# Kernel tuning notes

Measured on AMD Instinct MI355X. Metric: run time of the kernel, lower is better.

The kernel has to match this reference:

```python
import jax, jax.numpy as jnp
import numpy as np

N = 50000      # nodes
E = 800000     # edges (before self-loops)
F_IN = 128     # input features
HID = 64       # hidden width
CLS = 40       # classes
NEG_SLOPE = 0.2  # PyG GATConv default
EPS = 1e-16


def setup_inputs() -> dict:
    key = jax.random.key(0)
    ks = jax.random.split(key, 16)

    def lin(k, fi, fo):
        return jax.random.normal(k, (fi, fo), jnp.float32) / np.float32(np.sqrt(fi))

    def att(k, f):
        return jax.random.normal(k, (f,), jnp.float32) / np.float32(np.sqrt(f))

    return {
        "x": jax.random.normal(ks[0], (N, F_IN), jnp.float32),
        "edge_index": jax.random.randint(ks[1], (2, E), 0, N, dtype=jnp.int64),
        "W1": lin(ks[2], F_IN, HID), "a_src1": att(ks[3], HID), "a_dst1": att(ks[4], HID), "b1": jnp.zeros((HID,), jnp.float32),
        "W2": lin(ks[5], HID, HID),  "a_src2": att(ks[6], HID), "a_dst2": att(ks[7], HID), "b2": jnp.zeros((HID,), jnp.float32),
        "W3": lin(ks[8], HID, CLS),  "a_src3": att(ks[9], CLS), "a_dst3": att(ks[10], CLS), "b3": jnp.zeros((CLS,), jnp.float32),
    }


def gat_layer(x, src, dst, W, a_src, a_dst, b, n):
    # Single-head GATConv (PyG semantics, heads=1, add_self_loops already applied).
    h = x @ W                                  # [n, out]
    s_src = h @ a_src                          # [n]
    s_dst = h @ a_dst                          # [n]
    e = jax.nn.leaky_relu(s_src[src] + s_dst[dst], NEG_SLOPE)  # [E']
    # softmax over incoming edges of each destination node
    m = jax.ops.segment_max(e, dst, num_segments=n)            # [n]
    e = jnp.exp(e - m[dst])
    denom = jax.ops.segment_sum(e, dst, num_segments=n)        # [n]
    alpha = e / (denom[dst] + EPS)                             # [E']
    out = jax.ops.segment_sum(h[src] * alpha[:, None], dst, num_segments=n)
    return out + b


def reference(x, edge_index, W1, a_src1, a_dst1, b1, W2, a_src2, a_dst2, b2, W3, a_src3, a_dst3, b3):
    n = x.shape[0]
    loop = jnp.arange(n, dtype=edge_index.dtype)
    src = jnp.concatenate([edge_index[0], loop])   # add self-loops (GATConv default)
    dst = jnp.concatenate([edge_index[1], loop])

    h = gat_layer(x, src, dst, W1, a_src1, a_dst1, b1, n)
    h = jax.nn.gelu(h, approximate=False)          # torch F.gelu default = exact erf
    h = gat_layer(h, src, dst, W2, a_src2, a_dst2, b2, n)
    h = jax.nn.gelu(h, approximate=False)
    out = gat_layer(h, src, dst, W3, a_src3, a_dst3, b3, n)
    return out
```

## Files before the change

### kernel.cpp

```cpp
#include <hip/hip_runtime.h>
#include <hip/hip_bf16.h>
#include <math.h>


#define PAD_CAP 64
#define SCAT_BLOCKS 128

__device__ __forceinline__ int detect64(const int* __restrict__ ei) {
  int any = 0;
#pragma unroll
  for (int i = 1; i < 64; i += 2) any |= ei[i];
  return any == 0;
}

__device__ __forceinline__ void load_edge(const int* __restrict__ ei, int E,
                                          int e, int is64, int n, int& s,
                                          int& d) {
  if (is64) {
    s = ei[2 * e];
    d = ei[2 * (E + e)];
  } else {
    s = ei[e];
    d = ei[E + e];
  }
  s = min(max(s, 0), n - 1);
  d = min(max(d, 0), n - 1);
}


template <int F_IN, int F_OUT, bool SCATTER>
__global__ __launch_bounds__(256) void gemm_att(
    const float* __restrict__ x, const float* __restrict__ W,
    const float* __restrict__ a_src, const float* __restrict__ a_dst,
    __hip_bfloat16* __restrict__ h, float* __restrict__ s_src,
    float* __restrict__ s_dst, int n, const int* __restrict__ ei, int E,
    int* __restrict__ deg, int* __restrict__ col) {
  if constexpr (SCATTER) {
    if (blockIdx.x < SCAT_BLOCKS) {
      const int is64 = detect64(ei);
      const int total = E + n;
      const int stride = SCAT_BLOCKS * 256;
      int e = blockIdx.x * 256 + threadIdx.x;
      while (e < total) {
        int sv[8], dv[8], va[8], pos[8];
#pragma unroll
        for (int j = 0; j < 8; ++j) {
          const int ee = e + j * stride;
          va[j] = (ee < total);
          int s = 0, d = 0;
          if (va[j]) {
            if (ee < E) load_edge(ei, E, ee, is64, n, s, d);
            else { s = ee - E; d = ee - E; }
          }
          sv[j] = s;
          dv[j] = d;
        }
#pragma unroll
        for (int j = 0; j < 8; ++j)
          pos[j] = va[j] ? atomicAdd(deg + dv[j], 1) : PAD_CAP;
#pragma unroll
        for (int j = 0; j < 8; ++j)
          if (va[j] && pos[j] < PAD_CAP)
            col[((size_t)dv[j] << 6) + pos[j]] = sv[j];
        e += 8 * stride;
      }
      return;
    }
  }

  constexpr int TF = F_OUT / 4;
  __shared__ float Xt[F_IN * 65];
  __shared__ float red[2][4][64];
  const int wave = threadIdx.x >> 6, lane = threadIdx.x & 63;
  const int bid = SCATTER ? (int)blockIdx.x - SCAT_BLOCKS : (int)blockIdx.x;
  const int nb0 = bid * 64;
  const int node = nb0 + lane;

  {
    constexpr int Q = F_IN / 4;
    for (int i = threadIdx.x; i < 64 * Q; i += 256) {
      const int nd = i / Q, k4 = i % Q;
      float4 v = {0.f, 0.f, 0.f, 0.f};
      if (nb0 + nd < n)
        v = *(const float4*)(x + (size_t)(nb0 + nd) * F_IN + 4 * k4);
      Xt[(4 * k4 + 0) * 65 + nd] = v.x;
      Xt[(4 * k4 + 1) * 65 + nd] = v.y;
      Xt[(4 * k4 + 2) * 65 + nd] = v.z;
      Xt[(4 * k4 + 3) * 65 + nd] = v.w;
    }
  }
  __syncthreads();

  const int f0 = __builtin_amdgcn_readfirstlane(wave * TF);
  float acc[TF];
#pragma unroll
  for (int ff = 0; ff < TF; ++ff) acc[ff] = 0.f;

#pragma unroll 4
  for (int k = 0; k < F_IN; ++k) {
    const float xk = Xt[k * 65 + lane];
#pragma unroll
    for (int ff = 0; ff < TF; ++ff)
      acc[ff] = fmaf(xk, W[k * F_OUT + f0 + ff], acc[ff]);
  }

  float pa = 0.f, pb = 0.f;
#pragma unroll
  for (int ff = 0; ff < TF; ++ff) {
    pa = fmaf(acc[ff], a_src[f0 + ff], pa);
    pb = fmaf(acc[ff], a_dst[f0 + ff], pb);
  }
  if (node < n) {
#pragma unroll
    for (int ff = 0; ff < TF; ++ff)
      h[(size_t)node * F_OUT + f0 + ff] = __float2bfloat16(acc[ff]);
  }
  red[0][wave][lane] = pa;
  red[1][wave][lane] = pb;
  __syncthreads();
  if (wave == 0 && node < n) {
    s_src[node] = red[0][0][lane] + red[0][1][lane] + red[0][2][lane] +
                  red[0][3][lane];
    s_dst[node] = red[1][0][lane] + red[1][1][lane] + red[1][2][lane] +
                  red[1][3][lane];
  }
}

template <int F_OUT>
__global__ __launch_bounds__(1024) void aggr_gemm(
    const int* __restrict__ col, const int* __restrict__ deg_arr,
    const float* __restrict__ ssrc, const float* __restrict__ sdst,
    const __hip_bfloat16* __restrict__ h_in, const float* __restrict__ bias_in,
    const float* __restrict__ W, const float* __restrict__ a_src,
    const float* __restrict__ a_dst, __hip_bfloat16* __restrict__ h_out,
    float* __restrict__ ssrc_out, float* __restrict__ sdst_out, int n) {
  constexpr int F_IN = 64;
  constexpr int NW = F_OUT / 4;
  __shared__ float Xt[F_IN * 65];
  __shared__ float red[2][16][64];
  const int wave = threadIdx.x >> 6, lane = threadIdx.x & 63;
  const int q = lane >> 4, t4 = lane & 15;
  const int nb0 = blockIdx.x * 64;

  float4 bv = make_float4(0.f, 0.f, 0.f, 0.f);
  if (lane < 16) bv = *(const float4*)(bias_in + 4 * lane);

  const unsigned short* __restrict__ hu = (const unsigned short*)h_in + 4 * t4;

  for (int r = 0; r < 4; ++r) {
    const int dl = 4 * wave + r;
    const int d = nb0 + dl;
    float ax = 0.f, ay = 0.f, az = 0.f, aw_ = 0.f, inv = 0.f;
    if (d < n) {
      const int beg = d << 6;
      const int deg = min(deg_arr[d], PAD_CAP);
      const float sd = sdst[d];
      int s0 = 0;
      float w0 = 0.f;
      if (lane < deg) {
        s0 = col[beg + lane];
        float t = ssrc[s0] + sd;
        t = t > 0.f ? t : 0.2f * t;
        w0 = __expf(t);
      }
      float den = w0;
#pragma unroll
      for (int off = 32; off > 0; off >>= 1) den += __shfl_xor(den, off);
      inv = 1.f / (den + 1e-16f);

      int i = 0;
      for (; i + 16 <= deg; i += 16) {
        int ss[4];
        float ww[4];
        uint2 hv[4];
#pragma unroll
        for (int j = 0; j < 4; ++j) {
          ss[j] = __shfl(s0, i + 4 * j + q);
          ww[j] = __shfl(w0, i + 4 * j + q);
        }
#pragma unroll
        for (int j = 0; j < 4; ++j)
          hv[j] = *(const uint2*)(hu + (size_t)ss[j] * F_IN);
#pragma unroll
        for (int j = 0; j < 4; ++j) {
          ax = fmaf(ww[j], __uint_as_float(hv[j].x << 16), ax);
          ay = fmaf(ww[j], __uint_as_float(hv[j].x & 0xffff0000u), ay);
          az = fmaf(ww[j], __uint_as_float(hv[j].y << 16), az);
          aw_ = fmaf(ww[j], __uint_as_float(hv[j].y & 0xffff0000u), aw_);
        }
      }
      for (; i < deg; i += 4) {
        const int ss = __shfl(s0, i + q);
        const float ww = __shfl(w0, i + q);
        const uint2 hv = *(const uint2*)(hu + (size_t)ss * F_IN);
        ax = fmaf(ww, __uint_as_float(hv.x << 16), ax);
        ay = fmaf(ww, __uint_as_float(hv.x & 0xffff0000u), ay);
        az = fmaf(ww, __uint_as_float(hv.y << 16), az);
        aw_ = fmaf(ww, __uint_as_float(hv.y & 0xffff0000u), aw_);
      }
#pragma unroll
      for (int off = 32; off >= 16; off >>= 1) {
        ax += __shfl_xor(ax, off);
        ay += __shfl_xor(ay, off);
        az += __shfl_xor(az, off);
        aw_ += __shfl_xor(aw_, off);
      }
    }
    if (lane < 16) {
      float r0 = 0.f, r1 = 0.f, r2 = 0.f, r3 = 0.f;
      if (d < n) {
        r0 = ax * inv + bv.x;
        r1 = ay * inv + bv.y;
        r2 = az * inv + bv.z;
        r3 = aw_ * inv + bv.w;
        r0 = 0.5f * r0 * (1.f + erff(r0 * 0.70710678118654752f));
        r1 = 0.5f * r1 * (1.f + erff(r1 * 0.70710678118654752f));
        r2 = 0.5f * r2 * (1.f + erff(r2 * 0.70710678118654752f));
        r3 = 0.5f * r3 * (1.f + erff(r3 * 0.70710678118654752f));
      }
      Xt[(4 * lane + 0) * 65 + dl] = r0;
      Xt[(4 * lane + 1) * 65 + dl] = r1;
      Xt[(4 * lane + 2) * 65 + dl] = r2;
      Xt[(4 * lane + 3) * 65 + dl] = r3;
    }
  }
  __syncthreads();

  float pa = 0.f, pb = 0.f;
  const int node = nb0 + lane;
  if (wave < NW) {
    const int f0 = __builtin_amdgcn_readfirstlane(wave * 4);
    float acc[4] = {0.f, 0.f, 0.f, 0.f};
#pragma unroll 4
    for (int k = 0; k < F_IN; ++k) {
      const float xk = Xt[k * 65 + lane];
#pragma unroll
      for (int ff = 0; ff < 4; ++ff)
        acc[ff] = fmaf(xk, W[k * F_OUT + f0 + ff], acc[ff]);
    }
#pragma unroll
    for (int ff = 0; ff < 4; ++ff) {
      pa = fmaf(acc[ff], a_src[f0 + ff], pa);
      pb = fmaf(acc[ff], a_dst[f0 + ff], pb);
    }
    if (node < n) {
#pragma unroll
      for (int ff = 0; ff < 4; ++ff)
        h_out[(size_t)node * F_OUT + f0 + ff] = __float2bfloat16(acc[ff]);
    }
  }
  red[0][wave][lane] = pa;
  red[1][wave][lane] = pb;
  __syncthreads();
  if (wave == 0 && node < n) {
    float sa = 0.f, sb = 0.f;
#pragma unroll
    for (int w = 0; w < NW; ++w) {
      sa += red[0][w][lane];
      sb += red[1][w][lane];
    }
    ssrc_out[node] = sa;
    sdst_out[node] = sb;
  }
}

template <int F_OUT, bool GELU>
__global__ __launch_bounds__(256) void attn_aggr(
    const int* __restrict__ col, const int* __restrict__ deg_arr,
    const float* __restrict__ ssrc, const float* __restrict__ sdst,
    const __hip_bfloat16* __restrict__ h, const float* __restrict__ bias,
    float* __restrict__ out, int n) {
  constexpr int NF4 = (F_OUT + 3) / 4;
  const int wave = threadIdx.x >> 6, lane = threadIdx.x & 63;
  const int d = blockIdx.x * 4 + wave;
  if (d >= n) return;
  const int beg = d << 6;
  const int deg = min(deg_arr[d], PAD_CAP);
  const float sd = sdst[d];

  int s0 = 0;
  float w0 = 0.f;
  if (lane < deg) {
    s0 = col[beg + lane];
    float t = ssrc[s0] + sd;
    t = t > 0.f ? t : 0.2f * t;
    w0 = __expf(t);
  }
  float den = w0;
#pragma unroll
  for (int off = 32; off > 0; off >>= 1) den += __shfl_xor(den, off);
  const float inv = 1.f / (den + 1e-16f);

  const int q = lane >> 4, t4 = lane & 15;
  const bool act = (t4 < NF4);
  const unsigned short* __restrict__ hu = (const unsigned short*)h + 4 * t4;

  float ax = 0.f, ay = 0.f, az = 0.f, aw = 0.f;
  int i = 0;
  for (; i + 16 <= deg; i += 16) {
    int ss[4];
    float ww[4];
    uint2 hv[4];
#pragma unroll
    for (int j = 0; j < 4; ++j) {
      ss[j] = __shfl(s0, i + 4 * j + q);
      ww[j] = __shfl(w0, i + 4 * j + q);
    }
#pragma unroll
    for (int j = 0; j < 4; ++j) {
      hv[j].x = 0u;
      hv[j].y = 0u;
      if (act) hv[j] = *(const uint2*)(hu + (size_t)ss[j] * F_OUT);
    }
#pragma unroll
    for (int j = 0; j < 4; ++j) {
      ax = fmaf(ww[j], __uint_as_float(hv[j].x << 16), ax);
      ay = fmaf(ww[j], __uint_as_float(hv[j].x & 0xffff0000u), ay);
      az = fmaf(ww[j], __uint_as_float(hv[j].y << 16), az);
      aw = fmaf(ww[j], __uint_as_float(hv[j].y & 0xffff0000u), aw);
    }
  }
  for (; i < deg; i += 4) {
    const int ss = __shfl(s0, i + q);
    const float ww = __shfl(w0, i + q);
    uint2 hv;
    hv.x = 0u;
    hv.y = 0u;
    if (act) hv = *(const uint2*)(hu + (size_t)ss * F_OUT);
    ax = fmaf(ww, __uint_as_float(hv.x << 16), ax);
    ay = fmaf(ww, __uint_as_float(hv.x & 0xffff0000u), ay);
    az = fmaf(ww, __uint_as_float(hv.y << 16), az);
    aw = fmaf(ww, __uint_as_float(hv.y & 0xffff0000u), aw);
  }

#pragma unroll
  for (int off = 32; off >= 16; off >>= 1) {
    ax += __shfl_xor(ax, off);
    ay += __shfl_xor(ay, off);
    az += __shfl_xor(az, off);
    aw += __shfl_xor(aw, off);
  }

  if (lane < NF4) {
    const float4 bv = *(const float4*)(bias + 4 * lane);
    float r0 = ax * inv + bv.x;
    float r1 = ay * inv + bv.y;
    float r2 = az * inv + bv.z;
    float r3 = aw * inv + bv.w;
    if (GELU) {
      r0 = 0.5f * r0 * (1.f + erff(r0 * 0.70710678118654752f));
      r1 = 0.5f * r1 * (1.f + erff(r1 * 0.70710678118654752f));
      r2 = 0.5f * r2 * (1.f + erff(r2 * 0.70710678118654752f));
      r3 = 0.5f * r3 * (1.f + erff(r3 * 0.70710678118654752f));
    }
    *(float4*)(out + (size_t)d * F_OUT + 4 * lane) =
        make_float4(r0, r1, r2, r3);
  }
}

extern "C" void kernel_launch(void* const* d_in, const int* in_sizes, int n_in,
                              void* d_out, int out_size, void* d_ws,
                              size_t ws_size, hipStream_t stream) {
  const float* x = (const float*)d_in[0];
  const int* ei = (const int*)d_in[1];
  const float* W1 = (const float*)d_in[2];
  const float* as1 = (const float*)d_in[3];
  const float* ad1 = (const float*)d_in[4];
  const float* b1 = (const float*)d_in[5];
  const float* W2 = (const float*)d_in[6];
  const float* as2 = (const float*)d_in[7];
  const float* ad2 = (const float*)d_in[8];
  const float* b2 = (const float*)d_in[9];
  const float* W3 = (const float*)d_in[10];
  const float* as3 = (const float*)d_in[11];
  const float* ad3 = (const float*)d_in[12];
  const float* b3 = (const float*)d_in[13];

  const int n = in_sizes[0] / 128;
  const int E = in_sizes[1] / 2;

  const size_t need = ((size_t)n * (32 + 32 + 1 + 1 + 1 + 1 + 1 + PAD_CAP)) * 4 + 256;
  if (ws_size < need) return;

  __hip_bfloat16* hbA = (__hip_bfloat16*)d_ws;
  __hip_bfloat16* hbB = hbA + (size_t)n * 64;
  float* ssrcA = (float*)d_ws + (size_t)n * 64;
  float* sdstA = ssrcA + n;
  float* ssrcB = sdstA + n;
  float* sdstB = ssrcB + n;
  int* deg = (int*)(sdstB + n);
  int* col = deg + n;

  const int gemm_blocks = (n + 63) / 64;
  const int aggr_blocks = (n + 3) / 4;

  hipMemsetAsync(deg, 0, (size_t)n * 4, stream);
  gemm_att<128, 64, true><<<gemm_blocks + SCAT_BLOCKS, 256, 0, stream>>>(
      x, W1, as1, ad1, hbA, ssrcA, sdstA, n, ei, E, deg, col);

  aggr_gemm<64><<<gemm_blocks, 1024, 0, stream>>>(
      col, deg, ssrcA, sdstA, hbA, b1, W2, as2, ad2, hbB, ssrcB, sdstB, n);

  aggr_gemm<40><<<gemm_blocks, 1024, 0, stream>>>(
      col, deg, ssrcB, sdstB, hbB, b2, W3, as3, ad3, hbA, ssrcA, sdstA, n);

  attn_aggr<40, false><<<aggr_blocks, 256, 0, stream>>>(
      col, deg, ssrcA, sdstA, hbA, b3, (float*)d_out, n);
}
```

Measured before the change: 247.8 us.

## Batch per-node metadata loads and deepen gather prefetch in aggregation kernels

Both aggregation kernels now load degree, dst score, column indices and source scores for all four destination nodes a wave handles before doing any compute. This exposes more independent memory loads up front. The neighbor gather loop is restructured to issue up to six row loads per batch with a single guarded path instead of a 16-wide main loop plus tail. The final attn_aggr now processes four nodes per wave with fewer blocks, and launch-bounds occupancy hints are added. The trade-off is higher register pressure, which may limit occupancy.

```diff
diff --git a/kernel.cpp b/kernel.cpp
--- a/kernel.cpp
+++ b/kernel.cpp
@@ -5,6 +5,7 @@
 
 #define PAD_CAP 64
 #define SCAT_BLOCKS 128
+#define PF 6
 
 __device__ __forceinline__ int detect64(const int* __restrict__ ei) {
   int any = 0;
@@ -127,7 +128,7 @@
 }
 
 template <int F_OUT>
-__global__ __launch_bounds__(1024) void aggr_gemm(
+__global__ __launch_bounds__(1024, 2) void aggr_gemm(
     const int* __restrict__ col, const int* __restrict__ deg_arr,
     const float* __restrict__ ssrc, const float* __restrict__ sdst,
     const __hip_bfloat16* __restrict__ h_in, const float* __restrict__ bias_in,
@@ -147,64 +148,67 @@
 
   const unsigned short* __restrict__ hu = (const unsigned short*)h_in + 4 * t4;
 
+  int degv[4], s0v[4];
+  float sdv[4], svalv[4];
+#pragma unroll
+  for (int r = 0; r < 4; ++r) {
+    const int d = nb0 + 4 * wave + r;
+    const bool ok = d < n;
+    degv[r] = ok ? min(deg_arr[d], PAD_CAP) : 0;
+    sdv[r] = ok ? sdst[d] : 0.f;
+    s0v[r] = 0;
+    if (lane < degv[r]) s0v[r] = col[((size_t)d << 6) + lane];
+  }
+#pragma unroll
+  for (int r = 0; r < 4; ++r) {
+    svalv[r] = 0.f;
+    if (lane < degv[r]) svalv[r] = ssrc[s0v[r]];
+  }
+
+#pragma unroll
   for (int r = 0; r < 4; ++r) {
     const int dl = 4 * wave + r;
     const int d = nb0 + dl;
-    float ax = 0.f, ay = 0.f, az = 0.f, aw_ = 0.f, inv = 0.f;
-    if (d < n) {
-      const int beg = d << 6;
-      const int deg = min(deg_arr[d], PAD_CAP);
-      const float sd = sdst[d];
-      int s0 = 0;
-      float w0 = 0.f;
-      if (lane < deg) {
-        s0 = col[beg + lane];
-        float t = ssrc[s0] + sd;
-        t = t > 0.f ? t : 0.2f * t;
-        w0 = __expf(t);
-      }
-      float den = w0;
-#pragma unroll
-      for (int off = 32; off > 0; off >>= 1) den += __shfl_xor(den, off);
-      inv = 1.f / (den + 1e-16f);
-
-      int i = 0;
-      for (; i + 16 <= deg; i += 16) {
-        int ss[4];
-        float ww[4];
-        uint2 hv[4];
-#pragma unroll
-        for (int j = 0; j < 4; ++j) {
-          ss[j] = __shfl(s0, i + 4 * j + q);
-          ww[j] = __shfl(w0, i + 4 * j + q);
+    const int deg = degv[r];
+    float w0 = 0.f;
+    if (lane < deg) {
+      float t = svalv[r] + sdv[r];
+      t = t > 0.f ? t : 0.2f * t;
+      w0 = __expf(t);
+    }
+    float den = w0;
+#pragma unroll
+    for (int off = 32; off > 0; off >>= 1) den += __shfl_xor(den, off);
+    const float inv = 1.f / (den + 1e-16f);
+
+    float ax = 0.f, ay = 0.f, az = 0.f, aw_ = 0.f;
+    const int dg4 = (deg + 3) >> 2;
+    for (int base = 0; base < dg4; base += PF) {
+      const int rem = dg4 - base;
+      int ss[PF];
+      uint2 hv[PF];
+#pragma unroll
+      for (int j = 0; j < PF; ++j)
+        if (j < rem) ss[j] = __shfl(s0v[r], (base + j) * 4 + q);
+#pragma unroll
+      for (int j = 0; j < PF; ++j)
+        if (j < rem) hv[j] = *(const uint2*)(hu + (size_t)ss[j] * F_IN);
+#pragma unroll
+      for (int j = 0; j < PF; ++j)
+        if (j < rem) {
+          const float ww = __shfl(w0, (base + j) * 4 + q);
+          ax = fmaf(ww, __uint_as_float(hv[j].x << 16), ax);
+          ay = fmaf(ww, __uint_as_float(hv[j].x & 0xffff0000u), ay);
+          az = fmaf(ww, __uint_as_float(hv[j].y << 16), az);
+          aw_ = fmaf(ww, __uint_as_float(hv[j].y & 0xffff0000u), aw_);
         }
-#pragma unroll
-        for (int j = 0; j < 4; ++j)
-          hv[j] = *(const uint2*)(hu + (size_t)ss[j] * F_IN);
-#pragma unroll
-        for (int j = 0; j < 4; ++j) {
-          ax = fmaf(ww[j], __uint_as_float(hv[j].x << 16), ax);
-          ay = fmaf(ww[j], __uint_as_float(hv[j].x & 0xffff0000u), ay);
-          az = fmaf(ww[j], __uint_as_float(hv[j].y << 16), az);
-          aw_ = fmaf(ww[j], __uint_as_float(hv[j].y & 0xffff0000u), aw_);
-        }
-      }
-      for (; i < deg; i += 4) {
-        const int ss = __shfl(s0, i + q);
-        const float ww = __shfl(w0, i + q);
-        const uint2 hv = *(const uint2*)(hu + (size_t)ss * F_IN);
-        ax = fmaf(ww, __uint_as_float(hv.x << 16), ax);
-        ay = fmaf(ww, __uint_as_float(hv.x & 0xffff0000u), ay);
-        az = fmaf(ww, __uint_as_float(hv.y << 16), az);
-        aw_ = fmaf(ww, __uint_as_float(hv.y & 0xffff0000u), aw_);
-      }
-#pragma unroll
-      for (int off = 32; off >= 16; off >>= 1) {
-        ax += __shfl_xor(ax, off);
-        ay += __shfl_xor(ay, off);
-        az += __shfl_xor(az, off);
-        aw_ += __shfl_xor(aw_, off);
-      }
+    }
+#pragma unroll
+    for (int off = 32; off >= 16; off >>= 1) {
+      ax += __shfl_xor(ax, off);
+      ay += __shfl_xor(ay, off);
+      az += __shfl_xor(az, off);
+      aw_ += __shfl_xor(aw_, off);
     }
     if (lane < 16) {
       float r0 = 0.f, r1 = 0.f, r2 = 0.f, r3 = 0.f;
@@ -264,97 +268,97 @@
   }
 }
 
-template <int F_OUT, bool GELU>
-__global__ __launch_bounds__(256) void attn_aggr(
+template <int F_OUT>
+__global__ __launch_bounds__(256, 8) void attn_aggr(
     const int* __restrict__ col, const int* __restrict__ deg_arr,
     const float* __restrict__ ssrc, const float* __restrict__ sdst,
     const __hip_bfloat16* __restrict__ h, const float* __restrict__ bias,
     float* __restrict__ out, int n) {
   constexpr int NF4 = (F_OUT + 3) / 4;
   const int wave = threadIdx.x >> 6, lane = threadIdx.x & 63;
-  const int d = blockIdx.x * 4 + wave;
-  if (d >= n) return;
-  const int beg = d << 6;
-  const int deg = min(deg_arr[d], PAD_CAP);
-  const float sd = sdst[d];
-
-  int s0 = 0;
-  float w0 = 0.f;
-  if (lane < deg) {
-    s0 = col[beg + lane];
-    float t = ssrc[s0] + sd;
-    t = t > 0.f ? t : 0.2f * t;
-    w0 = __expf(t);
-  }
-  float den = w0;
-#pragma unroll
-  for (int off = 32; off > 0; off >>= 1) den += __shfl_xor(den, off);
-  const float inv = 1.f / (den + 1e-16f);
-
   const int q = lane >> 4, t4 = lane & 15;
+  const int d0 = (blockIdx.x * 4 + wave) * 4;
+  if (d0 >= n) return;
   const bool act = (t4 < NF4);
   const unsigned short* __restrict__ hu = (const unsigned short*)h + 4 * t4;
 
-  float ax = 0.f, ay = 0.f, az = 0.f, aw = 0.f;
-  int i = 0;
-  for (; i + 16 <= deg; i += 16) {
-    int ss[4];
-    float ww[4];
-    uint2 hv[4];
-#pragma unroll
-    for (int j = 0; j < 4; ++j) {
-      ss[j] = __shfl(s0, i + 4 * j + q);
-      ww[j] = __shfl(w0, i + 4 * j + q);
-    }
-#pragma unroll
-    for (int j = 0; j < 4; ++j) {
-      hv[j].x = 0u;
-      hv[j].y = 0u;
-      if (act) hv[j] = *(const uint2*)(hu + (size_t)ss[j] * F_OUT);
-    }
-#pragma unroll
-    for (int j = 0; j < 4; ++j) {
-      ax = fmaf(ww[j], __uint_as_float(hv[j].x << 16), ax);
-      ay = fmaf(ww[j], __uint_as_float(hv[j].x & 0xffff0000u), ay);
-      az = fmaf(ww[j], __uint_as_float(hv[j].y << 16), az);
-      aw = fmaf(ww[j], __uint_as_float(hv[j].y & 0xffff0000u), aw);
-    }
-  }
-  for (; i < deg; i += 4) {
-    const int ss = __shfl(s0, i + q);
-    const float ww = __shfl(w0, i + q);
-    uint2 hv;
-    hv.x = 0u;
-    hv.y = 0u;
-    if (act) hv = *(const uint2*)(hu + (size_t)ss * F_OUT);
-    ax = fmaf(ww, __uint_as_float(hv.x << 16), ax);
-    ay = fmaf(ww, __uint_as_float(hv.x & 0xffff0000u), ay);
-    az = fmaf(ww, __uint_as_float(hv.y << 16), az);
-    aw = fmaf(ww, __uint_as_float(hv.y & 0xffff0000u), aw);
-  }
-
-#pragma unroll
-  for (int off = 32; off >= 16; off >>= 1) {
-    ax += __shfl_xor(ax, off);
-    ay += __shfl_xor(ay, off);
-    az += __shfl_xor(az, off);
-    aw += __shfl_xor(aw, off);
-  }
-
-  if (lane < NF4) {
-    const float4 bv = *(const float4*)(bias + 4 * lane);
-    float r0 = ax * inv + bv.x;
-    float r1 = ay * inv + bv.y;
-    float r2 = az * inv + bv.z;
-    float r3 = aw * inv + bv.w;
-    if (GELU) {
-      r0 = 0.5f * r0 * (1.f + erff(r0 * 0.70710678118654752f));
-      r1 = 0.5f * r1 * (1.f + erff(r1 * 0.70710678118654752f));
-      r2 = 0.5f * r2 * (1.f + erff(r2 * 0.70710678118654752f));
-      r3 = 0.5f * r3 * (1.f + erff(r3 * 0.70710678118654752f));
-    }
-    *(float4*)(out + (size_t)d * F_OUT + 4 * lane) =
-        make_float4(r0, r1, r2, r3);
+  float4 bv = make_float4(0.f, 0.f, 0.f, 0.f);
+  if (lane < NF4) bv = *(const float4*)(bias + 4 * lane);
+
+  int degv[4], s0v[4];
+  float sdv[4], svalv[4];
+#pragma unroll
+  for (int r = 0; r < 4; ++r) {
+    const int d = d0 + r;
+    const bool ok = d < n;
+    degv[r] = ok ? min(deg_arr[d], PAD_CAP) : 0;
+    sdv[r] = ok ? sdst[d] : 0.f;
+    s0v[r] = 0;
+    if (lane < degv[r]) s0v[r] = col[((size_t)d << 6) + lane];
+  }
+#pragma unroll
+  for (int r = 0; r < 4; ++r) {
+    svalv[r] = 0.f;
+    if (lane < degv[r]) svalv[r] = ssrc[s0v[r]];
+  }
+
+#pragma unroll
+  for (int r = 0; r < 4; ++r) {
+    const int d = d0 + r;
+    const int deg = degv[r];
+    float w0 = 0.f;
+    if (lane < deg) {
+      float t = svalv[r] + sdv[r];
+      t = t > 0.f ? t : 0.2f * t;
+      w0 = __expf(t);
+    }
+    float den = w0;
+#pragma unroll
+    for (int off = 32; off > 0; off >>= 1) den += __shfl_xor(den, off);
+    const float inv = 1.f / (den + 1e-16f);
+
+    float ax = 0.f, ay = 0.f, az = 0.f, aw_ = 0.f;
+    const int dg4 = (deg + 3) >> 2;
+    for (int base = 0; base < dg4; base += PF) {
+      const int rem = dg4 - base;
+      int ss[PF];
+      uint2 hv[PF];
+#pragma unroll
+      for (int j = 0; j < PF; ++j)
+        if (j < rem) ss[j] = __shfl(s0v[r], (base + j) * 4 + q);
+#pragma unroll
+      for (int j = 0; j < PF; ++j)
+        if (j < rem) {
+          hv[j].x = 0u;
+          hv[j].y = 0u;
+          if (act) hv[j] = *(const uint2*)(hu + (size_t)ss[j] * F_OUT);
+        }
+#pragma unroll
+      for (int j = 0; j < PF; ++j)
+        if (j < rem) {
+          const float ww = __shfl(w0, (base + j) * 4 + q);
+          ax = fmaf(ww, __uint_as_float(hv[j].x << 16), ax);
+          ay = fmaf(ww, __uint_as_float(hv[j].x & 0xffff0000u), ay);
+          az = fmaf(ww, __uint_as_float(hv[j].y << 16), az);
+          aw_ = fmaf(ww, __uint_as_float(hv[j].y & 0xffff0000u), aw_);
+        }
+    }
+#pragma unroll
+    for (int off = 32; off >= 16; off >>= 1) {
+      ax += __shfl_xor(ax, off);
+      ay += __shfl_xor(ay, off);
+      az += __shfl_xor(az, off);
+      aw_ += __shfl_xor(aw_, off);
+    }
+
+    if (lane < NF4 && d < n) {
+      float r0 = ax * inv + bv.x;
+      float r1 = ay * inv + bv.y;
+      float r2 = az * inv + bv.z;
+      float r3 = aw_ * inv + bv.w;
+      *(float4*)(out + (size_t)d * F_OUT + 4 * lane) =
+          make_float4(r0, r1, r2, r3);
+    }
   }
 }
 
@@ -392,7 +396,7 @@
   int* col = deg + n;
 
   const int gemm_blocks = (n + 63) / 64;
-  const int aggr_blocks = (n + 3) / 4;
+  const int aggr3_blocks = (n + 15) / 16;
 
   hipMemsetAsync(deg, 0, (size_t)n * 4, stream);
   gemm_att<128, 64, true><<<gemm_blocks + SCAT_BLOCKS, 256, 0, stream>>>(
@@ -404,6 +408,6 @@
   aggr_gemm<40><<<gemm_blocks, 1024, 0, stream>>>(
       col, deg, ssrcB, sdstB, hbB, b2, W3, as3, ad3, hbA, ssrcA, sdstA, n);
 
-  attn_aggr<40, false><<<aggr_blocks, 256, 0, stream>>>(
+  attn_aggr<40><<<aggr3_blocks, 256, 0, stream>>>(
       col, deg, ssrcA, sdstA, hbA, b3, (float*)d_out, n);
 }
```

Measured after the change: 310.6 us. 25.4% more time.
